# Kernel tuning notes

Hardware: AMD Instinct MI355X
Metric: run time of the kernel (lower is better)

## Reference

```python
import jax, jax.numpy as jnp
import numpy as np

B, L, D, H, DH, MAX_SEQ = 2, 2048, 512, 8, 64, 2048


def setup_inputs() -> dict:
    key = jax.random.key(0)
    ks = jax.random.split(key, 9)
    w = 0.02
    return {
        "q": jax.random.normal(ks[0], (B, L, D), jnp.float32),
        "k": jax.random.normal(ks[1], (B, L, D), jnp.float32),
        "v": jax.random.normal(ks[2], (B, L, D), jnp.float32),
        "Wq_w": jax.random.normal(ks[3], (D, D), jnp.float32) * w,
        "Wq_b": jnp.zeros((D,), jnp.float32),
        "Wk_w": jax.random.normal(ks[4], (D, D), jnp.float32) * w,
        "Wk_b": jnp.zeros((D,), jnp.float32),
        "Wv_w": jax.random.normal(ks[5], (D, D), jnp.float32) * w,
        "Wv_b": jnp.zeros((D,), jnp.float32),
        "fc_w": jax.random.normal(ks[6], (D, D), jnp.float32) * w,
        "fc_b": jnp.zeros((D,), jnp.float32),
        "E": jax.random.normal(ks[7], (MAX_SEQ, DH), jnp.float32),
        "mask": jnp.triu(jnp.ones((L, L), jnp.int32), k=1)[None, None],  # 1 = masked
    }


def reference(q, k, v, Wq_w, Wq_b, Wk_w, Wk_b, Wv_w, Wv_b, fc_w, fc_b, E, mask):
    b, lq, d = q.shape

    def proj(x, w, bias):
        # torch Linear: x @ W.T + b, then split heads -> [b, h, l, dh]
        y = x @ w.T + bias
        return y.reshape(b, -1, H, DH).transpose(0, 2, 1, 3)

    qh, kh, vh = proj(q, Wq_w, Wq_b), proj(k, Wk_w, Wk_b), proj(v, Wv_w, Wv_b)
    len_q, len_k = qh.shape[2], kh.shape[2]

    # relative embedding slice (starting_point = max(0, max_seq - len_q))
    e = E[max(0, MAX_SEQ - len_q):, :]          # [m, dh], m == len_q here
    m = e.shape[0]

    QE = jnp.einsum('bhld,md->bhlm', qh, e)      # [b,h,lq,m]
    # qe_masking: keep column j of row i iff j >= m-1-i
    keep = (jnp.arange(m)[None, :] >= (m - 1 - jnp.arange(len_q))[:, None])
    QE = QE * keep.astype(QE.dtype)

    # skewing: left-pad last dim, reshape swapping trailing dims, drop first row
    padded = jnp.pad(QE, ((0, 0), (0, 0), (0, 0), (1, 0)))      # [b,h,lq,m+1]
    Srel = padded.reshape(b, H, m + 1, len_q)[:, :, 1:, :]       # [b,h,m,lq]
    if len_k > len_q:
        Srel = jnp.pad(Srel, ((0, 0), (0, 0), (0, len_k - len_q), (0, 0)))
    elif len_k < len_q:
        Srel = Srel[:, :, :, :len_k]

    QKt = jnp.einsum('bhld,bhmd->bhlm', qh, kh)                  # [b,h,lq,lk]
    logits = (QKt + Srel) / jnp.sqrt(jnp.float32(DH))
    logits = logits + mask.astype(logits.dtype) * jnp.float32(-1e9)
    attn = jax.nn.softmax(logits, axis=-1)
    out = jnp.einsum('bhlm,bhmd->bhld', attn, vh)                # [b,h,lq,dh]
    out = out.transpose(0, 2, 1, 3).reshape(b, len_q, d)
    out = out @ fc_w.T + fc_b
    return out, attn
```

## Files before the change

kernel.cpp:

```cpp
#include <hip/hip_runtime.h>
#include <hip/hip_bf16.h>
#include <cstdint>

typedef __bf16 bf16;
typedef __attribute__((ext_vector_type(8))) __bf16 bf16x8;
typedef __attribute__((ext_vector_type(4))) __bf16 bf16x4;
typedef __attribute__((ext_vector_type(4))) float f32x4;

#define MFMA16 __builtin_amdgcn_mfma_f32_16x16x32_bf16
#define MASKV (-1e30f)

static constexpr int Lq  = 2048;
static constexpr int BKt = 64;

__device__ __forceinline__ void async_load16(const void* g, void* l) {
  __builtin_amdgcn_global_load_lds(
      (__attribute__((address_space(1))) void*)g,
      (__attribute__((address_space(3))) void*)l, 16, 0, 0);
}

__device__ __forceinline__ unsigned pack2bf(float lo, float hi) {
  bf16 a = (bf16)lo, c = (bf16)hi;
  unsigned short ua, uc;
  __builtin_memcpy(&ua, &a, 2);
  __builtin_memcpy(&uc, &c, 2);
  return ((unsigned)uc << 16) | ua;
}

__global__ void convert_all(const float* __restrict__ q, const float* __restrict__ k,
                            const float* __restrict__ v, const float* __restrict__ wq,
                            const float* __restrict__ wk, const float* __restrict__ wv,
                            const float* __restrict__ fc, const float* __restrict__ E,
                            bf16* q_bf, bf16* k_bf, bf16* v_bf, bf16* wq_bf,
                            bf16* wk_bf, bf16* wv_bf, bf16* fc_bf, bf16* E_bf,
                            float* s_buf)
{
  int i = blockIdx.x * blockDim.x + threadIdx.x;
  const float* src; bf16* dst; int rel;
  if      (i < 524288)  { src = q;  dst = q_bf;  rel = i; }
  else if (i < 1048576) { src = k;  dst = k_bf;  rel = i - 524288; }
  else if (i < 1572864) { src = v;  dst = v_bf;  rel = i - 1048576; }
  else if (i < 1638400) { src = wq; dst = wq_bf; rel = i - 1572864; }
  else if (i < 1703936) { src = wk; dst = wk_bf; rel = i - 1638400; }
  else if (i < 1769472) { src = wv; dst = wv_bf; rel = i - 1703936; }
  else if (i < 1835008) { src = fc; dst = fc_bf; rel = i - 1769472; }
  else if (i < 1867776) { src = E;  dst = E_bf;  rel = i - 1835008; }
  else if (i < 1875968) {
    ((float4*)s_buf)[i - 1867776] = make_float4(0.f, 0.f, 0.f, 0.f);
    return;
  }
  else return;
  float4 x = *(const float4*)(src + (size_t)rel * 4);
  bf16x4 o;
  o[0] = (bf16)x.x; o[1] = (bf16)x.y; o[2] = (bf16)x.z; o[3] = (bf16)x.w;
  *(bf16x4*)(dst + (size_t)rel * 4) = o;
}

template<int MODE>
__device__ __forceinline__
void gemm512_core(const bf16* __restrict__ A, const bf16* __restrict__ Bm,
                  const float* __restrict__ bias, void* __restrict__ Cv,
                  int tm, int tn, char* lA, char* lB)
{
  const int tid = threadIdx.x, lane = tid & 63, wv = tid >> 6;
  const int wr = wv >> 1, wc = wv & 1;

  f32x4 acc[4][4];
#pragma unroll
  for (int m = 0; m < 4; ++m)
#pragma unroll
    for (int n = 0; n < 4; ++n) acc[m][n] = (f32x4){0.f, 0.f, 0.f, 0.f};

  for (int k0 = 0; k0 < 512; k0 += 64) {
    __syncthreads();
#pragma unroll
    for (int it = 0; it < 4; ++it) {
      int slot = it * 256 + wv * 64 + lane;
      int row = slot >> 3, c = slot & 7;
      int gk = k0 + ((c ^ (row & 7)) * 8);
      async_load16(A  + (size_t)(tm * 128 + row) * 512 + gk, lA + (it * 256 + wv * 64) * 16);
      async_load16(Bm + (size_t)(tn * 128 + row) * 512 + gk, lB + (it * 256 + wv * 64) * 16);
    }
    __syncthreads();
#pragma unroll
    for (int kc = 0; kc < 2; ++kc) {
      bf16x8 af[4], bfr[4];
#pragma unroll
      for (int m = 0; m < 4; ++m) {
        int row = wr * 64 + m * 16 + (lane & 15);
        int ch = ((lane >> 4) + kc * 4) ^ (row & 7);
        af[m] = *(const bf16x8*)(lA + row * 128 + ch * 16);
      }
#pragma unroll
      for (int n = 0; n < 4; ++n) {
        int row = wc * 64 + n * 16 + (lane & 15);
        int ch = ((lane >> 4) + kc * 4) ^ (row & 7);
        bfr[n] = *(const bf16x8*)(lB + row * 128 + ch * 16);
      }
#pragma unroll
      for (int m = 0; m < 4; ++m)
#pragma unroll
        for (int n = 0; n < 4; ++n)
          acc[m][n] = MFMA16(af[m], bfr[n], acc[m][n], 0, 0, 0);
    }
  }

#pragma unroll
  for (int m = 0; m < 4; ++m)
#pragma unroll
    for (int n = 0; n < 4; ++n)
#pragma unroll
      for (int r = 0; r < 4; ++r) {
        int gi = tm * 128 + wr * 64 + m * 16 + 4 * (lane >> 4) + r;
        int gj = tn * 128 + wc * 64 + n * 16 + (lane & 15);
        float vv = acc[m][n][r] + ((MODE == 2) ? bias[gi] : bias[gj]);
        if (MODE == 3) {
          ((float*)Cv)[(size_t)gi * 512 + gj] = vv;
        } else if (MODE == 2) {
          int h = gi >> 6, dh = gi & 63, b = gj >> 11, l = gj & 2047;
          ((bf16*)Cv)[((size_t)((b * 8 + h) * 64 + dh)) * 2048 + l] = (bf16)vv;
        } else {
          int b = gi >> 11, l = gi & 2047, h = gj >> 6, dh = gj & 63;
          ((bf16*)Cv)[((size_t)((b * 8 + h) * 2048 + l)) * 64 + dh] = (bf16)vv;
        }
      }
}

__global__ __launch_bounds__(256, 2)
void gemm_qkv(const bf16* __restrict__ q_bf, const bf16* __restrict__ k_bf,
              const bf16* __restrict__ v_bf, const bf16* __restrict__ wq_bf,
              const bf16* __restrict__ wk_bf, const bf16* __restrict__ wv_bf,
              const float* __restrict__ wq_b, const float* __restrict__ wk_b,
              const float* __restrict__ wv_b,
              bf16* __restrict__ qh, bf16* __restrict__ kh, bf16* __restrict__ vt)
{
  __shared__ __align__(16) char lA[16384];
  __shared__ __align__(16) char lB[16384];
  const int z = blockIdx.z;
  if (z == 0)      gemm512_core<0>(q_bf, wq_bf, wq_b, qh, blockIdx.x, blockIdx.y, lA, lB);
  else if (z == 1) gemm512_core<0>(k_bf, wk_bf, wk_b, kh, blockIdx.x, blockIdx.y, lA, lB);
  else             gemm512_core<2>(wv_bf, v_bf, wv_b, vt, blockIdx.y, blockIdx.x, lA, lB);
}

__global__ __launch_bounds__(256, 2)
void gemm_fc(const bf16* __restrict__ A, const bf16* __restrict__ Bm,
             const float* __restrict__ bias, float* __restrict__ Cv)
{
  __shared__ __align__(16) char lA[16384];
  __shared__ __align__(16) char lB[16384];
  gemm512_core<3>(A, Bm, bias, Cv, blockIdx.x, blockIdx.y, lA, lB);
}

__device__ __forceinline__ void stage_k(const bf16* __restrict__ kb, int j0,
                                        char* dst, int tid) {
#pragma unroll
  for (int it = 0; it < 2; ++it) {
    int slot = it * 256 + tid;
    int row = slot >> 3, c = slot & 7;
    async_load16(kb + (size_t)(j0 + row) * 64 + ((c ^ (row & 7)) * 8), dst + slot * 16);
  }
}
__device__ __forceinline__ void stage_v(const bf16* __restrict__ vb, int j0,
                                        char* dst, int tid) {
#pragma unroll
  for (int it = 0; it < 2; ++it) {
    int slot = it * 256 + tid;
    int row = slot >> 3, c = slot & 7;
    async_load16(vb + (size_t)row * Lq + j0 + ((c ^ (row & 7)) * 8), dst + slot * 16);
  }
}
__device__ __forceinline__ void stage_e(const bf16* __restrict__ Ebf, int rebase,
                                        char* dst, int tid) {
#pragma unroll
  for (int it = 0; it < 4; ++it) {
    int slot = it * 256 + tid;
    int t = slot >> 3, c = slot & 7;
    int re = rebase - t;
    re = re < 0 ? 0 : (re > 2047 ? 2047 : re);
    async_load16(Ebf + (size_t)re * 64 + ((c ^ (t & 7)) * 8), dst + slot * 16);
  }
}

__device__ __forceinline__ void attn_logits_sh(
    int i0, int j0, int wvx, int lane,
    const bf16x8 qf0, const bf16x8 qf1,
    const char* le, const char* lk, f32x4 acc_s[4])
{
  const int g = lane >> 4, b = lane & 15;
  f32x4 acc_t[5];
#pragma unroll
  for (int cf = 0; cf < 5; ++cf) {
    int t = wvx * 16 + cf * 16 + b;
    int c0 = g ^ (t & 7), c1 = (g + 4) ^ (t & 7);
    f32x4 a = (f32x4){0.f, 0.f, 0.f, 0.f};
    a = MFMA16(qf0, *(const bf16x8*)(le + t * 128 + c0 * 16), a, 0, 0, 0);
    a = MFMA16(qf1, *(const bf16x8*)(le + t * 128 + c1 * 16), a, 0, 0, 0);
    acc_t[cf] = a;
  }
#pragma unroll
  for (int cf = 0; cf < 4; ++cf) {
    int key = cf * 16 + b;
    int c0 = g ^ (key & 7);
    int c1 = (g + 4) ^ (key & 7);
    f32x4 a = (f32x4){0.f, 0.f, 0.f, 0.f};
    a = MFMA16(qf0, *(const bf16x8*)(lk + key * 128 + c0 * 16), a, 0, 0, 0);
    a = MFMA16(qf1, *(const bf16x8*)(lk + key * 128 + c1 * 16), a, 0, 0, 0);
    acc_s[cf] = a;
  }
  unsigned pr[4][4];
#pragma unroll
  for (int c = 0; c < 4; ++c)
#pragma unroll
    for (int r = 0; r < 4; ++r)
      pr[c][r] = pack2bf(acc_t[c][r], acc_t[c + 1][r]);

#pragma unroll
  for (int r = 0; r < 4; ++r) {
    const int qw  = 4 * g + r;
    const int sl  = (lane & 48) | ((63 + qw - b) & 15);
    const bool hi = qw > b;
#pragma unroll
    for (int cf = 0; cf < 4; ++cf) {
      unsigned u = __shfl(pr[3 - cf][r], sl);
      float t = hi ? __uint_as_float(u & 0xffff0000u)
                   : __uint_as_float(u << 16);
      float vv = (acc_s[cf][r] + t) * 0.125f;
      if (j0 + cf * 16 + b > i0 + wvx * 16 + qw) vv = MASKV;
      acc_s[cf][r] = vv;
    }
  }
}

__global__ __launch_bounds__(256, 2)
void produce(const bf16* __restrict__ qh, const bf16* __restrict__ kh,
             const bf16* __restrict__ vt, const bf16* __restrict__ Ebf,
             bf16* __restrict__ P_scr, float* __restrict__ O_slots,
             float* __restrict__ s_buf, float* __restrict__ attn_out)
{
  __shared__ __align__(16) char lds_k[2][64 * 128];
  __shared__ __align__(16) char lds_v[2][64 * 128];
  __shared__ __align__(16) char lds_e[2][128 * 128];
  __shared__ __align__(16) char lds_p[4][16 * 64 * 2];

  const int tid = threadIdx.x, lane = tid & 63, wvx = tid >> 6;
  const int n    = blockIdx.x;
  const int xcd  = n & 7;
  const int r0   = n >> 3;
  const int bh   = 2 * xcd + (r0 & 1);
  const int u    = r0 >> 1;
  const int f    = u & 7;
  const int qt   = 31 - (u >> 3);
  const int nc   = (qt >> 2) + 1;
  if (f >= nc) return;
  const int i0   = qt * 64;
  const int jbeg = f * 4;
  const int jend = (jbeg + 4 < qt + 1) ? jbeg + 4 : qt + 1;

  const bf16* qb = qh + (size_t)bh * Lq * 64;
  const bf16* kb = kh + (size_t)bh * Lq * 64;
  const bf16* vb = vt + (size_t)bh * 64 * Lq;
  float* attn_b = attn_out + (size_t)bh * Lq * Lq;
  bf16* P_b = P_scr + (size_t)bh * Lq * Lq;
  bf16* pst = (bf16*)lds_p[wvx];

  const int qrow = i0 + wvx * 16 + (lane & 15);
  const bf16x8 qf0 = *(const bf16x8*)(qb + (size_t)qrow * 64 + (lane >> 4) * 8);
  const bf16x8 qf1 = *(const bf16x8*)(qb + (size_t)qrow * 64 + 32 + (lane >> 4) * 8);

  f32x4 acc_s[4];
  f32x4 acc_o[4];
  float s_acc[4] = {0.f, 0.f, 0.f, 0.f};
#pragma unroll
  for (int nn = 0; nn < 4; ++nn) acc_o[nn] = (f32x4){0.f, 0.f, 0.f, 0.f};

  stage_k(kb, jbeg * BKt, lds_k[0], tid);
  stage_v(vb, jbeg * BKt, lds_v[0], tid);
  stage_e(Ebf, 2110 - i0 + jbeg * BKt, lds_e[0], tid);
  asm volatile("s_waitcnt vmcnt(0)" ::: "memory");
  __builtin_amdgcn_s_barrier();

  int lt = 0;
  for (int jt = jbeg; jt < jend; ++jt) {
    const int j0 = jt * BKt;
    const bool pre = (jt + 1 < jend);
    if (pre) {
      stage_k(kb, j0 + BKt, lds_k[lt ^ 1], tid);
      stage_v(vb, j0 + BKt, lds_v[lt ^ 1], tid);
      stage_e(Ebf, 2110 - i0 + j0 + BKt, lds_e[lt ^ 1], tid);
    }
    attn_logits_sh(i0, j0, wvx, lane, qf0, qf1, lds_e[lt], lds_k[lt], acc_s);
#pragma unroll
    for (int cf = 0; cf < 4; ++cf) {
      int kl = cf * 16 + (lane & 15);
      int chs = kl >> 3;
#pragma unroll
      for (int r = 0; r < 4; ++r) {
        int qw = 4 * (lane >> 4) + r;
        float p = __expf(acc_s[cf][r]);
        s_acc[r] += p;
        pst[qw * 64 + ((chs ^ (qw & 7)) * 8) + (kl & 7)] = (bf16)p;
      }
    }
    asm volatile("s_waitcnt lgkmcnt(0)" ::: "memory");
    __builtin_amdgcn_sched_barrier(0);
#pragma unroll
    for (int it = 0; it < 2; ++it) {
      int qw = it * 8 + (lane >> 3);
      int c = lane & 7;
      bf16x8 pv = *(const bf16x8*)(pst + qw * 64 + ((c ^ (qw & 7)) * 8));
      *(bf16x8*)(P_b + (size_t)(i0 + wvx * 16 + qw) * Lq + j0 + c * 8) = pv;
    }
    __builtin_amdgcn_s_setprio(1);
#pragma unroll
    for (int kc = 0; kc < 2; ++kc) {
      int qa = lane & 15;
      int cha = (kc * 4 + (lane >> 4)) ^ (qa & 7);
      bf16x8 pf = *(const bf16x8*)(pst + qa * 64 + cha * 8);
#pragma unroll
      for (int nn = 0; nn < 4; ++nn) {
        int dh = nn * 16 + (lane & 15);
        int chv = (kc * 4 + (lane >> 4)) ^ (dh & 7);
        bf16x8 vf = *(const bf16x8*)(lds_v[lt] + dh * 128 + chv * 16);
        acc_o[nn] = MFMA16(pf, vf, acc_o[nn], 0, 0, 0);
      }
    }
    __builtin_amdgcn_s_setprio(0);
    if (pre) {
      asm volatile("s_waitcnt vmcnt(2)" ::: "memory");
      __builtin_amdgcn_s_barrier();
      lt ^= 1;
    }
  }

  float* oslot = O_slots + (size_t)(((bh * 32 + qt) * 8 + f)) * 4096;
#pragma unroll
  for (int nn = 0; nn < 4; ++nn)
#pragma unroll
    for (int r = 0; r < 4; ++r) {
      int row = wvx * 16 + 4 * (lane >> 4) + r;
      oslot[row * 64 + nn * 16 + (lane & 15)] = acc_o[nn][r];
    }

#pragma unroll
  for (int r = 0; r < 4; ++r) {
    float s = s_acc[r];
    for (int d = 1; d < 16; d <<= 1) s += __shfl_xor(s, d);
    if ((lane & 15) == 0)
      atomicAdd(&s_buf[bh * Lq + i0 + wvx * 16 + 4 * (lane >> 4) + r], s);
  }

  for (int jz = qt + 1 + f; jz < 32; jz += nc) {
    const int j0 = jz * BKt;
#pragma unroll
    for (int kk = 0; kk < 4; ++kk) {
      int idx = kk * 256 + tid;
      int row = idx >> 4, c4 = idx & 15;
      float* p = attn_b + (size_t)(i0 + row) * Lq + j0 + c4 * 4;
      *(float4*)p = make_float4(0.f, 0.f, 0.f, 0.f);
    }
  }
}

__global__ __launch_bounds__(256, 8)
void finish(const bf16* __restrict__ P_scr, const float* __restrict__ s_buf,
            float* __restrict__ attn_out)
{
  const int lane = threadIdx.x & 63, wvx = threadIdx.x >> 6;
  const int row = blockIdx.x * 4 + wvx;
  const int i   = row & 2047;
  const int ncols = (i & ~63) + 64;
  const float inv = 1.f / s_buf[row];
  const bf16* src = P_scr + (size_t)row * Lq;
  float* dst = attn_out + (size_t)row * Lq;
  for (int c = lane * 4; c < ncols; c += 256) {
    bf16x4 pv = *(const bf16x4*)(src + c);
    float4 fo;
    fo.x = (float)pv[0] * inv;
    fo.y = (float)pv[1] * inv;
    fo.z = (float)pv[2] * inv;
    fo.w = (float)pv[3] * inv;
    *(float4*)(dst + c) = fo;
  }
}

__global__ void combine_o(const float* __restrict__ O_slots,
                          const float* __restrict__ s_buf, bf16* __restrict__ oh)
{
  const int sid = blockIdx.x;
  const int bh = sid >> 5, qt = sid & 31;
  const int nch = (qt >> 2) + 1;
  const float* base = O_slots + (size_t)(bh * 32 + qt) * 8 * 4096;
  const int b = bh >> 3, h = bh & 7;
  for (int e4 = threadIdx.x; e4 < 1024; e4 += 256) {
    float4 s = make_float4(0.f, 0.f, 0.f, 0.f);
    for (int ff = 0; ff < nch; ++ff) {
      float4 x = *(const float4*)(base + ff * 4096 + e4 * 4);
      s.x += x.x; s.y += x.y; s.z += x.z; s.w += x.w;
    }
    int row = e4 >> 4;
    int col = (e4 & 15) * 4;
    int ig = qt * 64 + row;
    float inv = 1.f / s_buf[bh * Lq + ig];
    bf16x4 o;
    o[0] = (bf16)(s.x * inv); o[1] = (bf16)(s.y * inv);
    o[2] = (bf16)(s.z * inv); o[3] = (bf16)(s.w * inv);
    *(bf16x4*)(oh + (size_t)(b * 2048 + ig) * 512 + h * 64 + col) = o;
  }
}

extern "C" void kernel_launch(void* const* d_in, const int* in_sizes, int n_in,
                              void* d_out, int out_size, void* d_ws, size_t ws_size,
                              hipStream_t stream) {
  const float* q    = (const float*)d_in[0];
  const float* k    = (const float*)d_in[1];
  const float* v    = (const float*)d_in[2];
  const float* wq   = (const float*)d_in[3];
  const float* wq_b = (const float*)d_in[4];
  const float* wk   = (const float*)d_in[5];
  const float* wk_b = (const float*)d_in[6];
  const float* wv   = (const float*)d_in[7];
  const float* wv_b = (const float*)d_in[8];
  const float* fc   = (const float*)d_in[9];
  const float* fc_b = (const float*)d_in[10];
  const float* E    = (const float*)d_in[11];

  if (ws_size < 233177088) return;
  char* ws = (char*)d_ws;
  bf16*  q_bf    = (bf16*)(ws);
  bf16*  k_bf    = (bf16*)(ws + 4194304);
  bf16*  v_bf    = (bf16*)(ws + 8388608);
  bf16*  wq_bf   = (bf16*)(ws + 12582912);
  bf16*  wk_bf   = (bf16*)(ws + 13107200);
  bf16*  wv_bf   = (bf16*)(ws + 13631488);
  bf16*  fc_bf   = (bf16*)(ws + 14155776);
  bf16*  E_bf    = (bf16*)(ws + 14680064);
  float* s_buf   = (float*)(ws + 14942208);
  bf16*  qh_bf   = (bf16*)(ws + 15073280);
  bf16*  kh_bf   = (bf16*)(ws + 19267584);
  bf16*  vt_bf   = (bf16*)(ws + 23461888);
  bf16*  oh_bf   = (bf16*)(ws + 27656192);
  float* O_slots = (float*)(ws + 31850496);
  bf16*  P_scr   = (bf16*)(ws + 98959360);

  float* out_f  = (float*)d_out;
  float* attn_f = out_f + 2097152;

  convert_all<<<7328, 256, 0, stream>>>(q, k, v, wq, wk, wv, fc, E,
      q_bf, k_bf, v_bf, wq_bf, wk_bf, wv_bf, fc_bf, E_bf, s_buf);
  gemm_qkv<<<dim3(32, 4, 3), 256, 0, stream>>>(q_bf, k_bf, v_bf,
      wq_bf, wk_bf, wv_bf, wq_b, wk_b, wv_b, qh_bf, kh_bf, vt_bf);
  produce<<<4096, 256, 0, stream>>>(qh_bf, kh_bf, vt_bf, E_bf,
                                    P_scr, O_slots, s_buf, attn_f);
  finish<<<8192, 256, 0, stream>>>(P_scr, s_buf, attn_f);
  combine_o<<<512, 256, 0, stream>>>(O_slots, s_buf, oh_bf);
  gemm_fc<<<dim3(32, 4), 256, 0, stream>>>(oh_bf, fc_bf, fc_b, out_f);
}
```

Baseline: 179.9 us.

## Stage relative-embedding E rows in a ring of aligned 64-row blocks

Replaces per-tile staging of 128 E rows, which overlap between consecutive key tiles, with a 4-slot ring buffer of 64-row aligned E blocks. Each iteration now loads only one new 64-row block instead of 128 rows, halving E global traffic and async load instructions per tile. The cost is more address arithmetic in the logits loop to find the ring slot and swizzle from the absolute row index. The prologue loads three blocks up front.

```diff
diff --git a/kernel.cpp b/kernel.cpp
--- a/kernel.cpp
+++ b/kernel.cpp
@@ -169,15 +169,16 @@
     async_load16(vb + (size_t)row * Lq + j0 + ((c ^ (row & 7)) * 8), dst + slot * 16);
   }
 }
-__device__ __forceinline__ void stage_e(const bf16* __restrict__ Ebf, int rebase,
-                                        char* dst, int tid) {
-#pragma unroll
-  for (int it = 0; it < 4; ++it) {
+__device__ __forceinline__ void stage_e_block(const bf16* __restrict__ Ebf, int block,
+                                              char* e_base, int tid) {
+  char* dst = e_base + (size_t)(block & 3) * 8192;
+#pragma unroll
+  for (int it = 0; it < 2; ++it) {
     int slot = it * 256 + tid;
-    int t = slot >> 3, c = slot & 7;
-    int re = rebase - t;
-    re = re < 0 ? 0 : (re > 2047 ? 2047 : re);
-    async_load16(Ebf + (size_t)re * 64 + ((c ^ (t & 7)) * 8), dst + slot * 16);
+    int row = slot >> 3, c = slot & 7;
+    int a = block * 64 + row;
+    int re = a < 0 ? 0 : (a > 2047 ? 2047 : a);
+    async_load16(Ebf + (size_t)re * 64 + ((c ^ (row & 7)) * 8), dst + slot * 16);
   }
 }
 
@@ -187,14 +188,18 @@
     const char* le, const char* lk, f32x4 acc_s[4])
 {
   const int g = lane >> 4, b = lane & 15;
+  const int rebase = 2110 - i0 + j0;
   f32x4 acc_t[5];
 #pragma unroll
   for (int cf = 0; cf < 5; ++cf) {
     int t = wvx * 16 + cf * 16 + b;
-    int c0 = g ^ (t & 7), c1 = (g + 4) ^ (t & 7);
+    int re = rebase - t;
+    re = re < 0 ? 0 : re;
+    int c0 = g ^ (re & 7), c1 = (g + 4) ^ (re & 7);
+    const char* ep = le + ((re >> 6) & 3) * 8192 + (re & 63) * 128;
     f32x4 a = (f32x4){0.f, 0.f, 0.f, 0.f};
-    a = MFMA16(qf0, *(const bf16x8*)(le + t * 128 + c0 * 16), a, 0, 0, 0);
-    a = MFMA16(qf1, *(const bf16x8*)(le + t * 128 + c1 * 16), a, 0, 0, 0);
+    a = MFMA16(qf0, *(const bf16x8*)(ep + c0 * 16), a, 0, 0, 0);
+    a = MFMA16(qf1, *(const bf16x8*)(ep + c1 * 16), a, 0, 0, 0);
     acc_t[cf] = a;
   }
 #pragma unroll
@@ -239,7 +244,7 @@
 {
   __shared__ __align__(16) char lds_k[2][64 * 128];
   __shared__ __align__(16) char lds_v[2][64 * 128];
-  __shared__ __align__(16) char lds_e[2][128 * 128];
+  __shared__ __align__(16) char lds_e[4 * 64 * 128];
   __shared__ __align__(16) char lds_p[4][16 * 64 * 2];
 
   const int tid = threadIdx.x, lane = tid & 63, wvx = tid >> 6;
@@ -273,9 +278,12 @@
 #pragma unroll
   for (int nn = 0; nn < 4; ++nn) acc_o[nn] = (f32x4){0.f, 0.f, 0.f, 0.f};
 
+  const int m0 = (2110 - i0 + jbeg * BKt) >> 6;
   stage_k(kb, jbeg * BKt, lds_k[0], tid);
   stage_v(vb, jbeg * BKt, lds_v[0], tid);
-  stage_e(Ebf, 2110 - i0 + jbeg * BKt, lds_e[0], tid);
+  stage_e_block(Ebf, m0 - 2, lds_e, tid);
+  stage_e_block(Ebf, m0 - 1, lds_e, tid);
+  stage_e_block(Ebf, m0,     lds_e, tid);
   asm volatile("s_waitcnt vmcnt(0)" ::: "memory");
   __builtin_amdgcn_s_barrier();
 
@@ -286,9 +294,9 @@
     if (pre) {
       stage_k(kb, j0 + BKt, lds_k[lt ^ 1], tid);
       stage_v(vb, j0 + BKt, lds_v[lt ^ 1], tid);
-      stage_e(Ebf, 2110 - i0 + j0 + BKt, lds_e[lt ^ 1], tid);
-    }
-    attn_logits_sh(i0, j0, wvx, lane, qf0, qf1, lds_e[lt], lds_k[lt], acc_s);
+      stage_e_block(Ebf, m0 + 1 + (jt - jbeg), lds_e, tid);
+    }
+    attn_logits_sh(i0, j0, wvx, lane, qf0, qf1, lds_e, lds_k[lt], acc_s);
 #pragma unroll
     for (int cf = 0; cf < 4; ++cf) {
       int kl = cf * 16 + (lane & 15);
```

New measurement: 182.2 us. Within noise of the previous version (+1.2%).
